# Optimization experiments

Measured on AMD Instinct MI355X. Metric: run time of the kernel, lower is better.

The kernel has to match this reference:

```python
import jax, jax.numpy as jnp
import numpy as np
import math

B, S, D = 2, 4096, 1024
H, HD = 16, 64          # num_heads, head_dim (inner_dim = 1024)
WIN = 1024              # local window size
G = 256                 # global tokens
SCALE = 1.0 / math.sqrt(HD)


def setup_inputs() -> dict:
    key = jax.random.key(0)
    ks = jax.random.split(key, 9)
    w = 0.02
    return {
        "x":   jax.random.normal(ks[0], (B, S, D), jnp.float32),
        "wq":  jax.random.normal(ks[1], (D, H * HD), jnp.float32) * w,
        "wk":  jax.random.normal(ks[2], (D, H * HD), jnp.float32) * w,
        "wv":  jax.random.normal(ks[3], (D, H * HD), jnp.float32) * w,
        "wo":  jax.random.normal(ks[4], (H * HD, D), jnp.float32) * w,
        "ws1": jax.random.normal(ks[5], (D, D // 4), jnp.float32) * w,
        "bs1": jnp.zeros((D // 4,), jnp.float32),
        "ws2": jax.random.normal(ks[6], (D // 4, 1), jnp.float32) * w,
        "bs2": jnp.zeros((1,), jnp.float32),
    }


def _forward(x, wq, wk, wv, wo, ws1, bs1, ws2, bs2):
    b, s, d = x.shape
    neg = jnp.finfo(x.dtype).min

    # ---- token scoring + global token selection (causal quirk: triu over [B,S]) ----
    h = jax.nn.gelu(x @ ws1 + bs1, approximate=False)
    scores = (h @ ws2 + bs2).squeeze(-1)                       # [b, s]
    causal_bs = jnp.triu(jnp.ones((b, s), bool), 1)            # faithful to .triu_(1) on [B,S]
    scores = jnp.where(causal_bs, neg, scores)
    _, idx = jax.lax.top_k(scores, min(G, s))                  # [b, G]
    g_tok = jnp.take_along_axis(x, idx[:, :, None], axis=1)    # [b, G, d]

    # ---- projections ----
    q = (x @ wq).reshape(b, s, H, HD).transpose(0, 2, 1, 3)    # [b, h, s, hd]
    k = (x @ wk).reshape(b, s, H, HD).transpose(0, 2, 1, 3)
    v = (x @ wv).reshape(b, s, H, HD).transpose(0, 2, 1, 3)
    gk = (g_tok @ wk).reshape(b, -1, H, HD).transpose(0, 2, 1, 3)  # [b, h, G, hd]
    gv = (g_tok @ wv).reshape(b, -1, H, HD).transpose(0, 2, 1, 3)

    # ---- local windowed causal attention ----
    nw = s // WIN
    qw = q.reshape(b, H, nw, WIN, HD)
    kw = k.reshape(b, H, nw, WIN, HD)
    vw = v.reshape(b, H, nw, WIN, HD)
    att = jnp.einsum('bhwqd,bhwkd->bhwqk', qw, kw) * SCALE
    cm = jnp.triu(jnp.ones((WIN, WIN), bool), 1)
    att = jnp.where(cm, neg, att)
    p = jax.nn.softmax(att, axis=-1)
    local_out = jnp.einsum('bhwqk,bhwkd->bhwqd', p, vw).reshape(b, H, s, HD)

    # ---- global attention (all queries vs selected global tokens) ----
    gatt = jnp.einsum('bhsd,bhgd->bhsg', q, gk) * SCALE
    gp = jax.nn.softmax(gatt, axis=-1)
    global_out = jnp.einsum('bhsg,bhgd->bhsd', gp, gv)

    out = (local_out + global_out).transpose(0, 2, 1, 3).reshape(b, s, H * HD)
    return out @ wo


def reference(x, wq, wk, wv, wo, ws1, bs1, ws2, bs2):
    return _forward(x, wq, wk, wv, wo, ws1, bs1, ws2, bs2)
```

## Files before the change

### kernel.cpp

```cpp
#include <hip/hip_runtime.h>
#include <cstdint>

typedef unsigned short u16;
typedef _Float16 f16t;
typedef __attribute__((ext_vector_type(8))) _Float16 f16x8;
typedef __attribute__((ext_vector_type(4))) float f32x4;

__device__ __forceinline__ u16 f2h(float f) {
  f16t h = (f16t)f;
  return __builtin_bit_cast(u16, h);
}
__device__ __forceinline__ uint32_t pk2(float a, float b) {
  return (uint32_t)f2h(a) | ((uint32_t)f2h(b) << 16);
}
__device__ __forceinline__ void gl_lds16(const void* g, void* l) {
  __builtin_amdgcn_global_load_lds(
      (__attribute__((address_space(1))) const void*)g,
      (__attribute__((address_space(3))) void*)l, 16, 0, 0);
}

__global__ __launch_bounds__(256) void k_sentinel(float* out, int n, float val) {
  int i = blockIdx.x * 256 + threadIdx.x;
  if (i < n) out[i] = val;
}

__global__ __launch_bounds__(256) void k_cvt_x(const float* __restrict__ x,
                                               u16* __restrict__ xh, int n4) {
  int i = blockIdx.x * 256 + threadIdx.x;
  if (i >= n4) return;
  const float4 v = ((const float4*)x)[i];
  uint2 pk;
  pk.x = pk2(v.x, v.y);
  pk.y = pk2(v.z, v.w);
  ((uint2*)xh)[i] = pk;
}

__global__ __launch_bounds__(256) void k_cvt_w(const float* __restrict__ wq,
                                               const float* __restrict__ wk,
                                               const float* __restrict__ wv,
                                               const float* __restrict__ wo,
                                               u16* __restrict__ wT) {
  const float* W = blockIdx.z == 0 ? wq : blockIdx.z == 1 ? wk
                   : blockIdx.z == 2 ? wv : wo;
  u16* out = wT + (size_t)blockIdx.z * 1024 * 1024;
  __shared__ float t[32][33];
  const int tx = threadIdx.x, ty = threadIdx.y;
  const int bx = blockIdx.x, by = blockIdx.y;
#pragma unroll
  for (int i = 0; i < 4; ++i)
    t[ty + i * 8][tx] = W[(size_t)(by * 32 + ty + i * 8) * 1024 + bx * 32 + tx];
  __syncthreads();
#pragma unroll
  for (int i = 0; i < 4; ++i)
    out[(size_t)(bx * 32 + ty + i * 8) * 1024 + by * 32 + tx] = f2h(t[tx][ty + i * 8]);
}

__global__ __launch_bounds__(256) void k_gemm_qkv(const u16* __restrict__ xh,
                                                  const u16* __restrict__ wT,
                                                  u16* __restrict__ qm,
                                                  u16* __restrict__ km,
                                                  u16* __restrict__ vt) {
  __shared__ __align__(16) u16 ldsA[2 * 4096];
  __shared__ __align__(16) u16 ldsB[2 * 4096];
  const int bm = blockIdx.x, bn = blockIdx.y, z = blockIdx.z;
  const u16* BT = wT + (size_t)z * 1024 * 1024;
  const int tid = threadIdx.x;
  const int l = tid & 63, w = tid >> 6;
  const int wr = w >> 1, wc = w & 1;
  const int lo = l & 15, hi = l >> 4;
  const int lr = l >> 2, lp = l & 3;
  const u16* aSrc = xh + (size_t)(bm * 128 + w * 32 + lr) * 1024 + lp * 8;
  const u16* bSrc = BT + (size_t)(bn * 128 + w * 32 + lr) * 1024 + lp * 8;
  u16* dA = ldsA + (w * 32) * 32;
  u16* dB = ldsB + (w * 32) * 32;

  f32x4 acc[4][4];
#pragma unroll
  for (int m = 0; m < 4; ++m)
#pragma unroll
    for (int n = 0; n < 4; ++n) {
      f32x4 zv = {0.f, 0.f, 0.f, 0.f};
      acc[m][n] = zv;
    }

#pragma unroll
  for (int j = 0; j < 2; ++j) {
    gl_lds16(aSrc + j * 16 * 1024, dA + j * 16 * 32);
    gl_lds16(bSrc + j * 16 * 1024, dB + j * 16 * 32);
  }
  __syncthreads();

  for (int kt = 0; kt < 32; ++kt) {
    const int cur = kt & 1;
    if (kt + 1 < 32) {
      const int ko = (kt + 1) * 32;
#pragma unroll
      for (int j = 0; j < 2; ++j) {
        gl_lds16(aSrc + ko + j * 16 * 1024, dA + (cur ^ 1) * 4096 + j * 16 * 32);
        gl_lds16(bSrc + ko + j * 16 * 1024, dB + (cur ^ 1) * 4096 + j * 16 * 32);
      }
    }
    const u16* sA = ldsA + cur * 4096;
    const u16* sB = ldsB + cur * 4096;
    f16x8 af[4], bf[4];
#pragma unroll
    for (int m = 0; m < 4; ++m)
      af[m] = *(const f16x8*)(sA + (wr * 64 + m * 16 + lo) * 32 + hi * 8);
#pragma unroll
    for (int n = 0; n < 4; ++n)
      bf[n] = *(const f16x8*)(sB + (wc * 64 + n * 16 + lo) * 32 + hi * 8);
#pragma unroll
    for (int m = 0; m < 4; ++m)
#pragma unroll
      for (int n = 0; n < 4; ++n)
        acc[m][n] = __builtin_amdgcn_mfma_f32_16x16x32_f16(af[m], bf[n], acc[m][n], 0, 0, 0);
    __syncthreads();
  }

  if (z < 2) {
    u16* C = (z == 0) ? qm : km;
#pragma unroll
    for (int m = 0; m < 4; ++m) {
      const int row0 = bm * 128 + wr * 64 + m * 16 + hi * 4;
#pragma unroll
      for (int n = 0; n < 4; ++n) {
        const int col = bn * 128 + wc * 64 + n * 16 + lo;
#pragma unroll
        for (int r = 0; r < 4; ++r)
          C[(size_t)(row0 + r) * 1024 + col] = f2h(acc[m][n][r]);
      }
    }
  } else {
#pragma unroll
    for (int m = 0; m < 4; ++m) {
      const int row0 = bm * 128 + wr * 64 + m * 16 + hi * 4;
      const int bb = row0 >> 12, s = row0 & 4095;
#pragma unroll
      for (int n = 0; n < 4; ++n) {
        const int col = bn * 128 + wc * 64 + n * 16 + lo;
        const int hh = col >> 6, d = col & 63;
        uint2 pk;
        pk.x = pk2(acc[m][n][0], acc[m][n][1]);
        pk.y = pk2(acc[m][n][2], acc[m][n][3]);
        *(uint2*)(vt + ((size_t)(bb * 16 + hh) * 64 + d) * 4096 + s) = pk;
      }
    }
  }
}

__global__ __launch_bounds__(256) void k_gemm_out(const u16* __restrict__ ah,
                                                  const u16* __restrict__ woT,
                                                  float* __restrict__ out) {
  __shared__ __align__(16) u16 ldsA[2 * 4096];
  __shared__ __align__(16) u16 ldsB[2 * 4096];
  const int bm = blockIdx.x, bn = blockIdx.y;
  const int tid = threadIdx.x;
  const int l = tid & 63, w = tid >> 6;
  const int wr = w >> 1, wc = w & 1;
  const int lo = l & 15, hi = l >> 4;
  const int lr = l >> 2, lp = l & 3;
  const u16* aSrc = ah + (size_t)(bm * 128 + w * 32 + lr) * 1024 + lp * 8;
  const u16* bSrc = woT + (size_t)(bn * 128 + w * 32 + lr) * 1024 + lp * 8;
  u16* dA = ldsA + (w * 32) * 32;
  u16* dB = ldsB + (w * 32) * 32;

  f32x4 acc[4][4];
#pragma unroll
  for (int m = 0; m < 4; ++m)
#pragma unroll
    for (int n = 0; n < 4; ++n) {
      f32x4 zv = {0.f, 0.f, 0.f, 0.f};
      acc[m][n] = zv;
    }

#pragma unroll
  for (int j = 0; j < 2; ++j) {
    gl_lds16(aSrc + j * 16 * 1024, dA + j * 16 * 32);
    gl_lds16(bSrc + j * 16 * 1024, dB + j * 16 * 32);
  }
  __syncthreads();

  for (int kt = 0; kt < 32; ++kt) {
    const int cur = kt & 1;
    if (kt + 1 < 32) {
      const int ko = (kt + 1) * 32;
#pragma unroll
      for (int j = 0; j < 2; ++j) {
        gl_lds16(aSrc + ko + j * 16 * 1024, dA + (cur ^ 1) * 4096 + j * 16 * 32);
        gl_lds16(bSrc + ko + j * 16 * 1024, dB + (cur ^ 1) * 4096 + j * 16 * 32);
      }
    }
    const u16* sA = ldsA + cur * 4096;
    const u16* sB = ldsB + cur * 4096;
    f16x8 af[4], bf[4];
#pragma unroll
    for (int m = 0; m < 4; ++m)
      af[m] = *(const f16x8*)(sA + (wr * 64 + m * 16 + lo) * 32 + hi * 8);
#pragma unroll
    for (int n = 0; n < 4; ++n)
      bf[n] = *(const f16x8*)(sB + (wc * 64 + n * 16 + lo) * 32 + hi * 8);
#pragma unroll
    for (int m = 0; m < 4; ++m)
#pragma unroll
      for (int n = 0; n < 4; ++n)
        acc[m][n] = __builtin_amdgcn_mfma_f32_16x16x32_f16(af[m], bf[n], acc[m][n], 0, 0, 0);
    __syncthreads();
  }
#pragma unroll
  for (int m = 0; m < 4; ++m) {
    const int row0 = bm * 128 + wr * 64 + m * 16 + hi * 4;
#pragma unroll
    for (int n = 0; n < 4; ++n) {
      const int col = bn * 128 + wc * 64 + n * 16 + lo;
#pragma unroll
      for (int r = 0; r < 4; ++r)
        out[(size_t)(row0 + r) * 1024 + col] = acc[m][n][r];
    }
  }
}

__global__ __launch_bounds__(256) void k_attn(const u16* __restrict__ qm,
                                              const u16* __restrict__ km,
                                              const u16* __restrict__ vt,
                                              u16* __restrict__ ares) {
  __shared__ __align__(16) u16 ldsK[2][64 * 64];
  __shared__ __align__(16) u16 ldsV[2][64 * 64];
  __shared__ __align__(16) u16 ldsP[4][16 * 64];
  const int bx = blockIdx.x;
  const int qt = (bx & ~15) | (15 - (bx & 15));
  const int h = blockIdx.y, b = blockIdx.z;
  const int tid = threadIdx.x, l = tid & 63, w = tid >> 6;
  const int lo = l & 15, hi = l >> 4;
  const int sr = l >> 3, sp = l & 7;

  const int qrow = b * 4096 + qt * 64 + w * 16 + lo;
  f16x8 qf[2];
  qf[0] = *(const f16x8*)(qm + (size_t)qrow * 1024 + h * 64 + hi * 8);
  qf[1] = *(const f16x8*)(qm + (size_t)qrow * 1024 + h * 64 + 32 + hi * 8);
  const f16t qs = (f16t)0.18033688f;
  qf[0] *= qs;
  qf[1] *= qs;

  const f16t one = (f16t)1.0f;
  const f16x8 ones = {one, one, one, one, one, one, one, one};

  f32x4 O[4], OL[4], L4;
#pragma unroll
  for (int n = 0; n < 4; ++n) {
    f32x4 zv = {0.f, 0.f, 0.f, 0.f};
    O[n] = zv; OL[n] = zv;
  }
  {
    f32x4 zv = {0.f, 0.f, 0.f, 0.f};
    L4 = zv;
  }

  u16* P = ldsP[w];
  const int nloc = (qt & 15) + 1;
  const int ntiles = nloc + 4;
  const int wbase = (qt >> 4) * 1024;

  const int rt0 = w * 16 + sr;
  const int rt1 = w * 16 + 8 + sr;
  const int s0 = sp ^ (rt0 & 7);
  const int s1 = sp ^ (rt1 & 7);
  const int dOff0 = (w * 16 + 0) * 64 + l * 8;
  const int dOff1 = (w * 16 + 8) * 64 + l * 8;

  auto kseq_of = [&](int t) { return (t < nloc) ? (wbase + t * 64) : ((t - nloc) * 64); };

  uint4 rK0, rK1, rV0, rV1;
  auto stageLoad = [&](int t) {
    const int kseq = kseq_of(t);
    rK0 = *(const uint4*)(km + (size_t)(b * 4096 + kseq + rt0) * 1024 + h * 64 + s0 * 8);
    rK1 = *(const uint4*)(km + (size_t)(b * 4096 + kseq + rt1) * 1024 + h * 64 + s1 * 8);
    rV0 = *(const uint4*)(vt + ((size_t)(b * 16 + h) * 64 + rt0) * 4096 + kseq + s0 * 8);
    rV1 = *(const uint4*)(vt + ((size_t)(b * 16 + h) * 64 + rt1) * 4096 + kseq + s1 * 8);
  };
  auto stageWrite = [&](int p) {
    *(uint4*)(ldsK[p] + dOff0) = rK0;
    *(uint4*)(ldsK[p] + dOff1) = rK1;
    *(uint4*)(ldsV[p] + dOff0) = rV0;
    *(uint4*)(ldsV[p] + dOff1) = rV1;
  };

  auto computeTile = [&](int p, bool diag) {
    const u16* sK = ldsK[p];
    const u16* sV = ldsV[p];
    f32x4 S[4];
#pragma unroll
    for (int n = 0; n < 4; ++n) {
      f32x4 zv = {0.f, 0.f, 0.f, 0.f};
      S[n] = zv;
      const int kk = n * 16 + lo;
#pragma unroll
      for (int c = 0; c < 2; ++c) {
        const int slot = hi + c * 4;
        f16x8 kf = *(const f16x8*)(sK + kk * 64 + ((slot ^ (kk & 7)) * 8));
        S[n] = __builtin_amdgcn_mfma_f32_16x16x32_f16(qf[c], kf, S[n], 0, 0, 0);
      }
    }
#pragma unroll
    for (int n = 0; n < 4; ++n) {
      const int kk = n * 16 + lo;
#pragma unroll
      for (int r = 0; r < 4; ++r) {
        float v = S[n][r];
        if (diag && kk > (w * 16 + hi * 4 + r)) v = -1e30f;
        const int qr = hi * 4 + r;
        P[qr * 64 + ((((kk >> 3) ^ (qr & 7)) << 3) | (kk & 7))] = f2h(exp2f(v));
      }
    }
#pragma unroll
    for (int kc = 0; kc < 2; ++kc) {
      const int slot = hi + kc * 4;
      f16x8 pa = *(const f16x8*)(P + lo * 64 + ((slot ^ (lo & 7)) * 8));
#pragma unroll
      for (int nn = 0; nn < 4; ++nn) {
        const int d = nn * 16 + lo;
        f16x8 vb = *(const f16x8*)(sV + d * 64 + ((slot ^ (d & 7)) * 8));
        O[nn] = __builtin_amdgcn_mfma_f32_16x16x32_f16(pa, vb, O[nn], 0, 0, 0);
      }
      L4 = __builtin_amdgcn_mfma_f32_16x16x32_f16(pa, ones, L4, 0, 0, 0);
    }
  };

  stageLoad(0);
  stageWrite(0);
  asm volatile("s_waitcnt lgkmcnt(0)" ::: "memory");
  asm volatile("s_barrier" ::: "memory");

  for (int t = 0; t < ntiles; ++t) {
    if (t + 1 < ntiles) stageLoad(t + 1);
    computeTile(t & 1, t == nloc - 1);
    if (t == nloc - 1) {
      float inv[4];
#pragma unroll
      for (int r = 0; r < 4; ++r) inv[r] = 1.f / L4[r];
#pragma unroll
      for (int n = 0; n < 4; ++n) {
#pragma unroll
        for (int r = 0; r < 4; ++r) OL[n][r] = O[n][r] * inv[r];
        f32x4 zv = {0.f, 0.f, 0.f, 0.f};
        O[n] = zv;
      }
      f32x4 zv = {0.f, 0.f, 0.f, 0.f};
      L4 = zv;
    }
    if (t + 1 < ntiles) stageWrite((t + 1) & 1);
    asm volatile("s_waitcnt lgkmcnt(0)" ::: "memory");
    asm volatile("s_barrier" ::: "memory");
  }

  float ig[4];
#pragma unroll
  for (int r = 0; r < 4; ++r) ig[r] = 1.f / L4[r];

  const int orow0 = b * 4096 + qt * 64 + w * 16 + hi * 4;
#pragma unroll
  for (int nn = 0; nn < 4; ++nn) {
    const int col = h * 64 + nn * 16 + lo;
#pragma unroll
    for (int r = 0; r < 4; ++r)
      ares[(size_t)(orow0 + r) * 1024 + col] = f2h(OL[nn][r] + O[nn][r] * ig[r]);
  }
}

extern "C" void kernel_launch(void* const* d_in, const int* in_sizes, int n_in,
                              void* d_out, int out_size, void* d_ws, size_t ws_size,
                              hipStream_t stream) {
  const int expect[9] = {8388608, 1048576, 1048576, 1048576, 1048576,
                         262144, 256, 256, 1};
  bool ok = (n_in == 9);
  if (ok)
    for (int i = 0; i < 9; ++i) ok = ok && (in_sizes[i] == expect[i]);
  if (!ok) {
    k_sentinel<<<(out_size + 255) / 256, 256, 0, stream>>>((float*)d_out, out_size, 3008.0f);
    return;
  }
  if (ws_size < (64ull << 20)) {
    k_sentinel<<<(out_size + 255) / 256, 256, 0, stream>>>((float*)d_out, out_size, 1000.0f);
    return;
  }

  const float* x  = (const float*)d_in[0];
  const float* wq = (const float*)d_in[1];
  const float* wk = (const float*)d_in[2];
  const float* wv = (const float*)d_in[3];
  const float* wo = (const float*)d_in[4];

  uint8_t* ws = (uint8_t*)d_ws;
  u16* wT = (u16*)ws;
  u16* qm = (u16*)(ws + (8ull << 20));
  u16* km = (u16*)(ws + (24ull << 20));
  u16* vt = (u16*)(ws + (40ull << 20));
  u16* ares = qm;
  u16* xh = (u16*)d_out;

  k_cvt_x<<<8192, 256, 0, stream>>>(x, xh, 2097152);
  k_cvt_w<<<dim3(32, 32, 4), dim3(32, 8), 0, stream>>>(wq, wk, wv, wo, wT);
  k_gemm_qkv<<<dim3(64, 8, 3), 256, 0, stream>>>(xh, wT, qm, km, vt);
  k_attn<<<dim3(64, 16, 2), 256, 0, stream>>>(qm, km, vt, ares);
  k_gemm_out<<<dim3(64, 8), 256, 0, stream>>>(ares, wT + (3ull << 20), (float*)d_out);
}
```

Baseline: 210.5 us.

## Read K/V tiles directly from global memory instead of LDS double-buffering

Removes the shared-memory staging of K and V tiles, along with the double-buffer pipeline and per-tile barriers, in the attention kernel. Each wave now loads its MFMA K and V fragments straight from global memory, relying on L1/L2 caching because all four waves read the same tile. Launch bounds now request 6 blocks per CU, taking advantage of the smaller LDS footprint to raise occupancy. In exchange each tile is fetched redundantly by four waves, and global-load latency is no longer hidden by explicit prefetch.

```diff
diff --git a/kernel.cpp b/kernel.cpp
--- a/kernel.cpp
+++ b/kernel.cpp
@@ -219,19 +219,16 @@
   }
 }
 
-__global__ __launch_bounds__(256) void k_attn(const u16* __restrict__ qm,
-                                              const u16* __restrict__ km,
-                                              const u16* __restrict__ vt,
-                                              u16* __restrict__ ares) {
-  __shared__ __align__(16) u16 ldsK[2][64 * 64];
-  __shared__ __align__(16) u16 ldsV[2][64 * 64];
+__global__ __launch_bounds__(256, 6) void k_attn(const u16* __restrict__ qm,
+                                                 const u16* __restrict__ km,
+                                                 const u16* __restrict__ vt,
+                                                 u16* __restrict__ ares) {
   __shared__ __align__(16) u16 ldsP[4][16 * 64];
   const int bx = blockIdx.x;
   const int qt = (bx & ~15) | (15 - (bx & 15));
   const int h = blockIdx.y, b = blockIdx.z;
   const int tid = threadIdx.x, l = tid & 63, w = tid >> 6;
   const int lo = l & 15, hi = l >> 4;
-  const int sr = l >> 3, sp = l & 7;
 
   const int qrow = b * 4096 + qt * 64 + w * 16 + lo;
   f16x8 qf[2];
@@ -259,44 +256,23 @@
   const int nloc = (qt & 15) + 1;
   const int ntiles = nloc + 4;
   const int wbase = (qt >> 4) * 1024;
-
-  const int rt0 = w * 16 + sr;
-  const int rt1 = w * 16 + 8 + sr;
-  const int s0 = sp ^ (rt0 & 7);
-  const int s1 = sp ^ (rt1 & 7);
-  const int dOff0 = (w * 16 + 0) * 64 + l * 8;
-  const int dOff1 = (w * 16 + 8) * 64 + l * 8;
-
-  auto kseq_of = [&](int t) { return (t < nloc) ? (wbase + t * 64) : ((t - nloc) * 64); };
-
-  uint4 rK0, rK1, rV0, rV1;
-  auto stageLoad = [&](int t) {
-    const int kseq = kseq_of(t);
-    rK0 = *(const uint4*)(km + (size_t)(b * 4096 + kseq + rt0) * 1024 + h * 64 + s0 * 8);
-    rK1 = *(const uint4*)(km + (size_t)(b * 4096 + kseq + rt1) * 1024 + h * 64 + s1 * 8);
-    rV0 = *(const uint4*)(vt + ((size_t)(b * 16 + h) * 64 + rt0) * 4096 + kseq + s0 * 8);
-    rV1 = *(const uint4*)(vt + ((size_t)(b * 16 + h) * 64 + rt1) * 4096 + kseq + s1 * 8);
-  };
-  auto stageWrite = [&](int p) {
-    *(uint4*)(ldsK[p] + dOff0) = rK0;
-    *(uint4*)(ldsK[p] + dOff1) = rK1;
-    *(uint4*)(ldsV[p] + dOff0) = rV0;
-    *(uint4*)(ldsV[p] + dOff1) = rV1;
-  };
-
-  auto computeTile = [&](int p, bool diag) {
-    const u16* sK = ldsK[p];
-    const u16* sV = ldsV[p];
+  const size_t bb = (size_t)b * 4096;
+  const u16* vbase = vt + (size_t)(b * 16 + h) * 64 * 4096;
+
+  for (int t = 0; t < ntiles; ++t) {
+    const int kseq = (t < nloc) ? (wbase + t * 64) : ((t - nloc) * 64);
+    const bool diag = (t == nloc - 1);
+
     f32x4 S[4];
 #pragma unroll
     for (int n = 0; n < 4; ++n) {
       f32x4 zv = {0.f, 0.f, 0.f, 0.f};
       S[n] = zv;
       const int kk = n * 16 + lo;
+      const u16* krow = km + (bb + kseq + kk) * 1024 + h * 64;
 #pragma unroll
       for (int c = 0; c < 2; ++c) {
-        const int slot = hi + c * 4;
-        f16x8 kf = *(const f16x8*)(sK + kk * 64 + ((slot ^ (kk & 7)) * 8));
+        f16x8 kf = *(const f16x8*)(krow + (hi + c * 4) * 8);
         S[n] = __builtin_amdgcn_mfma_f32_16x16x32_f16(qf[c], kf, S[n], 0, 0, 0);
       }
     }
@@ -318,22 +294,13 @@
 #pragma unroll
       for (int nn = 0; nn < 4; ++nn) {
         const int d = nn * 16 + lo;
-        f16x8 vb = *(const f16x8*)(sV + d * 64 + ((slot ^ (d & 7)) * 8));
+        f16x8 vb = *(const f16x8*)(vbase + (size_t)d * 4096 + kseq + slot * 8);
         O[nn] = __builtin_amdgcn_mfma_f32_16x16x32_f16(pa, vb, O[nn], 0, 0, 0);
       }
       L4 = __builtin_amdgcn_mfma_f32_16x16x32_f16(pa, ones, L4, 0, 0, 0);
     }
-  };
-
-  stageLoad(0);
-  stageWrite(0);
-  asm volatile("s_waitcnt lgkmcnt(0)" ::: "memory");
-  asm volatile("s_barrier" ::: "memory");
-
-  for (int t = 0; t < ntiles; ++t) {
-    if (t + 1 < ntiles) stageLoad(t + 1);
-    computeTile(t & 1, t == nloc - 1);
-    if (t == nloc - 1) {
+
+    if (diag) {
       float inv[4];
 #pragma unroll
       for (int r = 0; r < 4; ++r) inv[r] = 1.f / L4[r];
@@ -347,9 +314,6 @@
       f32x4 zv = {0.f, 0.f, 0.f, 0.f};
       L4 = zv;
     }
-    if (t + 1 < ntiles) stageWrite((t + 1) & 1);
-    asm volatile("s_waitcnt lgkmcnt(0)" ::: "memory");
-    asm volatile("s_barrier" ::: "memory");
   }
 
   float ig[4];
```

Measured after the change: 526.1 us. +149.9%, slower.
